# Kernel optimization log

Measured on AMD Instinct MI355X. Metric: run time of the kernel, lower is better.

Reference implementation:

```python
import jax, jax.numpy as jnp
import numpy as np


def setup_inputs() -> dict:
    key = jax.random.key(0)
    k1, k2 = jax.random.split(key)
    B, S, D, K = 16, 2048, 256, 512
    features = jax.random.normal(k1, (B, S, D), dtype=jnp.float32)
    Ck = jax.random.normal(k2, (1, K, D), dtype=jnp.float32)
    return {"features": features, "Ck": Ck}


def reference(features, Ck):
    # features: (B, S, D); Ck: (1, K, D)
    # Squared euclidean distance to each of K centers: (B, S, K)
    # Computed as ||f||^2 + ||c||^2 - 2 f.c to avoid the (B*S, K, D) diff tensor.
    C = Ck[0]                                   # (K, D)
    f_sq = jnp.sum(features * features, axis=-1, keepdims=True)   # (B, S, 1)
    c_sq = jnp.sum(C * C, axis=-1)                                # (K,)
    cross = jnp.einsum("bsd,kd->bsk", features, C)               # (B, S, K)
    return f_sq + c_sq[None, None, :] - 2.0 * cross
```

## Files before the change

kernel.cpp:

```cpp
#include <hip/hip_runtime.h>

typedef __attribute__((ext_vector_type(8))) short bf16x8;
typedef __attribute__((ext_vector_type(4))) float f32x4;

#define NCH 8

__device__ inline unsigned short f2bf(float f) {
  unsigned int u = __builtin_bit_cast(unsigned int, f);
  u += 0x7fffu + ((u >> 16) & 1u);
  return (unsigned short)(u >> 16);
}

__device__ inline void gload16(const void* g, void* l) {
  __builtin_amdgcn_global_load_lds(
      (const __attribute__((address_space(1))) void*)g,
      (__attribute__((address_space(3))) void*)l, 16, 0, 0);
}

__global__ void prep_c(const float* __restrict__ C, unsigned short* __restrict__ Cbf,
                       float* __restrict__ csq, int K) {
  const int w = threadIdx.x >> 6, lane = threadIdx.x & 63;
  const int row = blockIdx.x * 4 + w;
  if (row >= K) return;
  const float4 v = *reinterpret_cast<const float4*>(&C[(size_t)row * 256 + lane * 4]);
  ushort4 b;
  b.x = f2bf(v.x); b.y = f2bf(v.y); b.z = f2bf(v.z); b.w = f2bf(v.w);
  const int boff = (lane * 8) ^ ((row & 7) << 4);
  *reinterpret_cast<ushort4*>((char*)Cbf + (size_t)row * 512 + boff) = b;
  float sq = v.x * v.x + v.y * v.y + v.z * v.z + v.w * v.w;
#pragma unroll
  for (int o = 32; o; o >>= 1) sq += __shfl_xor(sq, o);
  if (lane == 0) csq[row] = sq;
}

__global__ __launch_bounds__(256, 4) void dist_fused(
    const float* __restrict__ F, const unsigned short* __restrict__ Cbf,
    const float* __restrict__ csq, float* __restrict__ out, int M, int N) {
  __shared__ __align__(16) char Bs[2][32 * 512];
  __shared__ __align__(16) float csq_s[256];

  const int t = threadIdx.x;
  const int w = t >> 6, l = t & 63;
  const int rl = l & 15, kh = l >> 4;
  const int amask = (rl & 7) << 4;

  const int workid = (blockIdx.x & 7) * 128 + (blockIdx.x >> 3);
  const int m0 = (workid >> 1) * 64;
  const int n0 = (workid & 1) * 256;
  const int mrow = m0 + w * 16 + rl;

  const int srow = t >> 5;
  const int scol = (t & 31) * 16;
  const char* Bsrc = (const char*)Cbf + (size_t)(n0 + srow) * 512 + scol;

#define STAGE(CH, BUF)                                                        \
  {                                                                           \
    _Pragma("unroll")                                                         \
    for (int j = 0; j < 4; ++j)                                               \
      gload16(Bsrc + (size_t)(CH) * 16384 + j * 4096,                         \
              (char*)Bs[BUF] + j * 4096 + t * 16);                            \
  }

  STAGE(0, 0)
  if (t < 64)
    gload16((const char*)csq + (size_t)n0 * 4 + t * 16, (char*)csq_s + t * 16);

  const char* Arow = (const char*)F + (size_t)mrow * 1024 + kh * 32;
  f32x4 a0[8], a1[8];
#pragma unroll
  for (int kt = 0; kt < 8; ++kt) {
    a0[kt] = *reinterpret_cast<const f32x4*>(Arow + kt * 128);
    a1[kt] = *reinterpret_cast<const f32x4*>(Arow + kt * 128 + 16);
  }

  bf16x8 af[8];
  float rsq = 0.f;
#pragma unroll
  for (int kt = 0; kt < 8; ++kt) {
    const f32x4 x = a0[kt], y = a1[kt];
    rsq += x[0] * x[0] + x[1] * x[1] + x[2] * x[2] + x[3] * x[3] +
           y[0] * y[0] + y[1] * y[1] + y[2] * y[2] + y[3] * y[3];
    bf16x8 v;
    v[0] = (short)f2bf(x[0]); v[1] = (short)f2bf(x[1]);
    v[2] = (short)f2bf(x[2]); v[3] = (short)f2bf(x[3]);
    v[4] = (short)f2bf(y[0]); v[5] = (short)f2bf(y[1]);
    v[6] = (short)f2bf(y[2]); v[7] = (short)f2bf(y[3]);
    af[kt] = v;
    asm volatile("" : "+v"(af[kt]));
  }
  float fv = rsq;
  fv += __shfl_xor(fv, 16);
  fv += __shfl_xor(fv, 32);

  asm volatile("s_waitcnt vmcnt(0)" ::: "memory");
  __builtin_amdgcn_s_barrier();
  asm volatile("" ::: "memory");

#pragma unroll
  for (int c = 0; c < NCH; ++c) {
    const int cur = c & 1;
    if (c < NCH - 1) {
      STAGE(c + 1, cur ^ 1)
      asm volatile("s_waitcnt vmcnt(4)" ::: "memory");
    } else {
      asm volatile("s_waitcnt vmcnt(0)" ::: "memory");
    }
    __builtin_amdgcn_s_barrier();
    asm volatile("" ::: "memory");

#pragma unroll
    for (int ni = 0; ni < 2; ++ni) {
      f32x4 acc = (f32x4){0.f, 0.f, 0.f, 0.f};
#pragma unroll
      for (int kt = 0; kt < 8; ++kt) {
        const bf16x8 bfr = *reinterpret_cast<const bf16x8*>(
            (const char*)Bs[cur] + (ni * 16 + rl) * 512 + ((kt * 64 + kh * 16) ^ amask));
        acc = __builtin_amdgcn_mfma_f32_16x16x32_bf16(bfr, af[kt], acc, 0, 0, 0);
      }
      const int nloc = c * 32 + ni * 16 + kh * 4;
      const float4 cs4 = *reinterpret_cast<const float4*>(
          (const char*)csq_s + (size_t)nloc * 4);
      float4 v;
      v.x = fv + cs4.x - 2.0f * acc[0];
      v.y = fv + cs4.y - 2.0f * acc[1];
      v.z = fv + cs4.z - 2.0f * acc[2];
      v.w = fv + cs4.w - 2.0f * acc[3];
      *reinterpret_cast<float4*>(&out[(size_t)mrow * N + n0 + nloc]) = v;
    }

    __builtin_amdgcn_s_barrier();
    asm volatile("" ::: "memory");
  }
}

extern "C" void kernel_launch(void* const* d_in, const int* in_sizes, int n_in,
                              void* d_out, int out_size, void* d_ws, size_t ws_size,
                              hipStream_t stream) {
  const float* F = (const float*)d_in[0];
  const float* C = (const float*)d_in[1];
  float* out = (float*)d_out;
  const int D = 256;
  const int M = in_sizes[0] / D;
  const int N = in_sizes[1] / D;

  unsigned short* Cbf = (unsigned short*)d_ws;
  float* csq = (float*)(Cbf + (size_t)N * D);

  hipLaunchKernelGGL(prep_c, dim3(N / 4), dim3(256), 0, stream, C, Cbf, csq, N);
  const int nwg = (M / 64) * 2;
  hipLaunchKernelGGL(dist_fused, dim3(nwg), dim3(256), 0, stream,
                     F, Cbf, csq, out, M, N);
}
```

Measured before the change: 34.05 us.

## Shrink tiles to 64x64 and drop the double-buffered B pipeline

Each workgroup now computes a 64x64 output tile instead of 64x256. The whole 64-row bf16 C tile is loaded into LDS once, so the chunked double-buffered staging and per-chunk barriers go away. The c-squared values are read straight from global memory rather than staged in LDS, and the A loads are split into two halves to cut register pressure. The trade-off is four times as many workgroups, with each one re-reading and re-converting its fp32 feature rows, which multiplies global reads of F by four.

```diff
diff --git a/kernel.cpp b/kernel.cpp
--- a/kernel.cpp
+++ b/kernel.cpp
@@ -2,8 +2,6 @@
 
 typedef __attribute__((ext_vector_type(8))) short bf16x8;
 typedef __attribute__((ext_vector_type(4))) float f32x4;
-
-#define NCH 8
 
 __device__ inline unsigned short f2bf(float f) {
   unsigned int u = __builtin_bit_cast(unsigned int, f);
@@ -36,57 +34,49 @@
 __global__ __launch_bounds__(256, 4) void dist_fused(
     const float* __restrict__ F, const unsigned short* __restrict__ Cbf,
     const float* __restrict__ csq, float* __restrict__ out, int M, int N) {
-  __shared__ __align__(16) char Bs[2][32 * 512];
-  __shared__ __align__(16) float csq_s[256];
+  __shared__ __align__(16) char Bs[64 * 512];
 
   const int t = threadIdx.x;
   const int w = t >> 6, l = t & 63;
   const int rl = l & 15, kh = l >> 4;
   const int amask = (rl & 7) << 4;
 
-  const int workid = (blockIdx.x & 7) * 128 + (blockIdx.x >> 3);
-  const int m0 = (workid >> 1) * 64;
-  const int n0 = (workid & 1) * 256;
+  const int work = (blockIdx.x & 7) * 512 + (blockIdx.x >> 3);
+  const int m0 = (work >> 3) * 64;
+  const int n0 = (work & 7) * 64;
   const int mrow = m0 + w * 16 + rl;
 
   const int srow = t >> 5;
   const int scol = (t & 31) * 16;
   const char* Bsrc = (const char*)Cbf + (size_t)(n0 + srow) * 512 + scol;
-
-#define STAGE(CH, BUF)                                                        \
-  {                                                                           \
-    _Pragma("unroll")                                                         \
-    for (int j = 0; j < 4; ++j)                                               \
-      gload16(Bsrc + (size_t)(CH) * 16384 + j * 4096,                         \
-              (char*)Bs[BUF] + j * 4096 + t * 16);                            \
-  }
-
-  STAGE(0, 0)
-  if (t < 64)
-    gload16((const char*)csq + (size_t)n0 * 4 + t * 16, (char*)csq_s + t * 16);
+#pragma unroll
+  for (int j = 0; j < 8; ++j)
+    gload16(Bsrc + (size_t)j * 4096, (char*)Bs + j * 4096 + t * 16);
 
   const char* Arow = (const char*)F + (size_t)mrow * 1024 + kh * 32;
-  f32x4 a0[8], a1[8];
-#pragma unroll
-  for (int kt = 0; kt < 8; ++kt) {
-    a0[kt] = *reinterpret_cast<const f32x4*>(Arow + kt * 128);
-    a1[kt] = *reinterpret_cast<const f32x4*>(Arow + kt * 128 + 16);
-  }
-
   bf16x8 af[8];
   float rsq = 0.f;
 #pragma unroll
-  for (int kt = 0; kt < 8; ++kt) {
-    const f32x4 x = a0[kt], y = a1[kt];
-    rsq += x[0] * x[0] + x[1] * x[1] + x[2] * x[2] + x[3] * x[3] +
-           y[0] * y[0] + y[1] * y[1] + y[2] * y[2] + y[3] * y[3];
-    bf16x8 v;
-    v[0] = (short)f2bf(x[0]); v[1] = (short)f2bf(x[1]);
-    v[2] = (short)f2bf(x[2]); v[3] = (short)f2bf(x[3]);
-    v[4] = (short)f2bf(y[0]); v[5] = (short)f2bf(y[1]);
-    v[6] = (short)f2bf(y[2]); v[7] = (short)f2bf(y[3]);
-    af[kt] = v;
-    asm volatile("" : "+v"(af[kt]));
+  for (int h = 0; h < 2; ++h) {
+    f32x4 a0[4], a1[4];
+#pragma unroll
+    for (int k = 0; k < 4; ++k) {
+      a0[k] = *reinterpret_cast<const f32x4*>(Arow + (h * 4 + k) * 128);
+      a1[k] = *reinterpret_cast<const f32x4*>(Arow + (h * 4 + k) * 128 + 16);
+    }
+#pragma unroll
+    for (int k = 0; k < 4; ++k) {
+      const f32x4 x = a0[k], y = a1[k];
+      rsq += x[0] * x[0] + x[1] * x[1] + x[2] * x[2] + x[3] * x[3] +
+             y[0] * y[0] + y[1] * y[1] + y[2] * y[2] + y[3] * y[3];
+      bf16x8 v;
+      v[0] = (short)f2bf(x[0]); v[1] = (short)f2bf(x[1]);
+      v[2] = (short)f2bf(x[2]); v[3] = (short)f2bf(x[3]);
+      v[4] = (short)f2bf(y[0]); v[5] = (short)f2bf(y[1]);
+      v[6] = (short)f2bf(y[2]); v[7] = (short)f2bf(y[3]);
+      af[h * 4 + k] = v;
+      asm volatile("" : "+v"(af[h * 4 + k]));
+    }
   }
   float fv = rsq;
   fv += __shfl_xor(fv, 16);
@@ -97,39 +87,22 @@
   asm volatile("" ::: "memory");
 
 #pragma unroll
-  for (int c = 0; c < NCH; ++c) {
-    const int cur = c & 1;
-    if (c < NCH - 1) {
-      STAGE(c + 1, cur ^ 1)
-      asm volatile("s_waitcnt vmcnt(4)" ::: "memory");
-    } else {
-      asm volatile("s_waitcnt vmcnt(0)" ::: "memory");
+  for (int ni = 0; ni < 4; ++ni) {
+    f32x4 acc = (f32x4){0.f, 0.f, 0.f, 0.f};
+#pragma unroll
+    for (int kt = 0; kt < 8; ++kt) {
+      const bf16x8 bfr = *reinterpret_cast<const bf16x8*>(
+          (const char*)Bs + (ni * 16 + rl) * 512 + ((kt * 64 + kh * 16) ^ amask));
+      acc = __builtin_amdgcn_mfma_f32_16x16x32_bf16(bfr, af[kt], acc, 0, 0, 0);
     }
-    __builtin_amdgcn_s_barrier();
-    asm volatile("" ::: "memory");
-
-#pragma unroll
-    for (int ni = 0; ni < 2; ++ni) {
-      f32x4 acc = (f32x4){0.f, 0.f, 0.f, 0.f};
-#pragma unroll
-      for (int kt = 0; kt < 8; ++kt) {
-        const bf16x8 bfr = *reinterpret_cast<const bf16x8*>(
-            (const char*)Bs[cur] + (ni * 16 + rl) * 512 + ((kt * 64 + kh * 16) ^ amask));
-        acc = __builtin_amdgcn_mfma_f32_16x16x32_bf16(bfr, af[kt], acc, 0, 0, 0);
-      }
-      const int nloc = c * 32 + ni * 16 + kh * 4;
-      const float4 cs4 = *reinterpret_cast<const float4*>(
-          (const char*)csq_s + (size_t)nloc * 4);
-      float4 v;
-      v.x = fv + cs4.x - 2.0f * acc[0];
-      v.y = fv + cs4.y - 2.0f * acc[1];
-      v.z = fv + cs4.z - 2.0f * acc[2];
-      v.w = fv + cs4.w - 2.0f * acc[3];
-      *reinterpret_cast<float4*>(&out[(size_t)mrow * N + n0 + nloc]) = v;
-    }
-
-    __builtin_amdgcn_s_barrier();
-    asm volatile("" ::: "memory");
+    const int nloc = n0 + ni * 16 + kh * 4;
+    const float4 cs4 = *reinterpret_cast<const float4*>(&csq[nloc]);
+    float4 v;
+    v.x = fv + cs4.x - 2.0f * acc[0];
+    v.y = fv + cs4.y - 2.0f * acc[1];
+    v.z = fv + cs4.z - 2.0f * acc[2];
+    v.w = fv + cs4.w - 2.0f * acc[3];
+    *reinterpret_cast<float4*>(&out[(size_t)mrow * N + nloc]) = v;
   }
 }
 
@@ -147,7 +120,7 @@
   float* csq = (float*)(Cbf + (size_t)N * D);
 
   hipLaunchKernelGGL(prep_c, dim3(N / 4), dim3(256), 0, stream, C, Cbf, csq, N);
-  const int nwg = (M / 64) * 2;
+  const int nwg = (M / 64) * (N / 64);
   hipLaunchKernelGGL(dist_fused, dim3(nwg), dim3(256), 0, stream,
                      F, Cbf, csq, out, M, N);
 }
```

Result: slower. 51.98 us (+52.7%).
